# Kernel optimization log

Measured on AMD Instinct MI355X. Metric: run time of the kernel, lower is better.

Reference implementation:

```python
import jax, jax.numpy as jnp
import numpy as np

D_MODEL = 1024
N_HEADS = 16
D_K = D_MODEL // N_HEADS
B, S = 2, 2048


def setup_inputs() -> dict:
    key = jax.random.key(0)
    ks = jax.random.split(key, 5)
    sc = 1.0 / np.sqrt(D_MODEL)
    return {
        "x": jax.random.normal(ks[0], (B, S, D_MODEL), dtype=jnp.float32),
        "W_qkv": jax.random.normal(ks[1], (D_MODEL, 3 * D_MODEL), dtype=jnp.float32) * sc,
        "b_qkv": jnp.zeros((3 * D_MODEL,), dtype=jnp.float32),
        "W_out": jax.random.normal(ks[2], (D_MODEL, D_MODEL), dtype=jnp.float32) * sc,
        "b_out": jnp.zeros((D_MODEL,), dtype=jnp.float32),
    }


def reference(x, W_qkv, b_qkv, W_out, b_out):
    Bb, Ss, _ = x.shape
    qkv = x @ W_qkv + b_qkv                     # [B,S,3*D]
    qkv = qkv.reshape(Bb, Ss, 3, N_HEADS, D_K)
    qkv = jnp.transpose(qkv, (2, 0, 3, 1, 4))   # [3,B,H,S,Dk]
    q, k, v = qkv[0], qkv[1], qkv[2]
    scale = jnp.asarray(np.sqrt(D_K), dtype=x.dtype)
    attn = jnp.einsum('bhsd,bhtd->bhst', q, k) / scale  # [B,H,S,S]
    attn = jax.nn.softmax(attn, axis=-1)
    out = jnp.einsum('bhst,bhtd->bhsd', attn, v)        # [B,H,S,Dk]
    out = jnp.transpose(out, (0, 2, 1, 3)).reshape(Bb, Ss, D_MODEL)
    return out @ W_out + b_out
```

## Files before the change

### kernel.cpp

```cpp
#include <hip/hip_runtime.h>

typedef __bf16 bf16x8 __attribute__((ext_vector_type(8)));
typedef __bf16 bf16x4 __attribute__((ext_vector_type(4)));
typedef __bf16 bf16x2 __attribute__((ext_vector_type(2)));
typedef float f32x4 __attribute__((ext_vector_type(4)));
typedef unsigned short u16;
typedef unsigned short u16x4 __attribute__((ext_vector_type(4)));
typedef unsigned int u32;
typedef unsigned int u32x2 __attribute__((ext_vector_type(2)));
typedef unsigned int u32x4 __attribute__((ext_vector_type(4)));

__device__ __forceinline__ u16 f2bu(float f) {
  __bf16 h = (__bf16)f;
  return __builtin_bit_cast(u16, h);
}

__device__ __forceinline__ void gld16(const u16* g, const __bf16* lds) {
  __builtin_amdgcn_global_load_lds(
      (const __attribute__((address_space(1))) u32*)(uintptr_t)g,
      (__attribute__((address_space(3))) u32*)(u32)(uintptr_t)lds, 16, 0, 0);
}

__device__ __forceinline__ void tr_tile(const float* __restrict__ in, u16* __restrict__ out,
                                        int R, int C, int bx, int by, int tid) {
  __shared__ u16 t[64][65];
  int tx = tid & 63, ty = tid >> 6;
  int r0 = by * 64, c0 = bx * 64;
  for (int i = 0; i < 16; ++i)
    t[ty + i * 4][tx] = f2bu(in[(size_t)(r0 + ty + i * 4) * C + c0 + tx]);
  __syncthreads();
  for (int i = 0; i < 16; ++i)
    out[(size_t)(c0 + ty + i * 4) * R + r0 + tx] = t[tx][ty + i * 4];
}

__global__ __launch_bounds__(256) void prep(const float* __restrict__ Wqkv,
                                            u16* __restrict__ Wqkv_t,
                                            const float* __restrict__ Wout,
                                            u16* __restrict__ Wout_t,
                                            const float* __restrict__ x,
                                            u16* __restrict__ xb) {
  int id = blockIdx.x, tid = threadIdx.x;
  if (id < 768) {
    tr_tile(Wqkv, Wqkv_t, 1024, 3072, id % 48, id / 48, tid);
  } else if (id < 1024) {
    int id2 = id - 768;
    tr_tile(Wout, Wout_t, 1024, 1024, id2 % 16, id2 / 16, tid);
  } else {
    size_t i = ((size_t)(id - 1024) * 256 + tid) * 8;
    f32x4 a0 = *(const f32x4*)(x + i);
    f32x4 a1 = *(const f32x4*)(x + i + 4);
    bf16x8 v;
    for (int j = 0; j < 4; ++j) { v[j] = (__bf16)a0[j]; v[j + 4] = (__bf16)a1[j]; }
    *(bf16x8*)(xb + i) = v;
  }
}

template <int MODE, int TM, int TN, int MT, int NT, int XM, int XN>
__global__ __launch_bounds__(256) void gemm_bt(const u16* __restrict__ A,
                                               const u16* __restrict__ Bt,
                                               const float* __restrict__ bias,
                                               void* __restrict__ O0v,
                                               u16* __restrict__ O1,
                                               u16* __restrict__ O2,
                                               int M, int N, int K) {
  constexpr int NI = TM / 32;
  constexpr int NJ = TN / 32;
  constexpr int AE = TM * 32;
  constexpr int BE = TN * 32;
  __shared__ __bf16 smem[2 * (AE + BE)];

  int tid = threadIdx.x;
  int w = tid >> 6, lane = tid & 63, quad = lane >> 4, l16 = lane & 15;
  int wr = w >> 1, wc = w & 1;

  int id = blockIdx.x;
  int xcd = id & 7, s0i = id >> 3;
  int mg = xcd % (MT / XM), ng = xcd / (MT / XM);
  int sm = s0i % XM, sn = s0i / XM;
  int m0 = (mg * XM + sm) * TM, n0 = (ng * XN + sn) * TN;

  int srow = w * 16 + (lane >> 2);
  int sch = (lane & 3) ^ ((lane >> 3) & 3);
  const u16* Ag = A + (size_t)(m0 + srow) * K + sch * 8;
  const u16* Bg = Bt + (size_t)(n0 + srow) * K + sch * 8;

  int swl = (quad ^ ((l16 >> 1) & 3)) << 3;

  f32x4 acc[NI][NJ] = {};

#define GLD_STEP(c, kk)                                                          \
  {                                                                              \
    for (int p = 0; p < TM / 64; ++p)                                            \
      gld16(Ag + (size_t)p * 64 * K + (kk), smem + (c) * (AE + BE) + w * 512 + p * 2048); \
    for (int p = 0; p < TN / 64; ++p)                                            \
      gld16(Bg + (size_t)p * 64 * K + (kk), smem + (c) * (AE + BE) + AE + w * 512 + p * 2048); \
  }

  GLD_STEP(0, 0);
  int NS = K / 32;
  for (int s = 0; s < NS; ++s) {
    int cur = s & 1;
    __syncthreads();
    if (s + 1 < NS) GLD_STEP(1 - cur, (s + 1) * 32);
    const __bf16* Asub = smem + cur * (AE + BE);
    const __bf16* Bsub = Asub + AE;
    bf16x8 af[NI], bfr[NJ];
    for (int i = 0; i < NI; ++i)
      af[i] = *(const bf16x8*)(Asub + (wr * (TM / 2) + i * 16 + l16) * 32 + swl);
    for (int j = 0; j < NJ; ++j)
      bfr[j] = *(const bf16x8*)(Bsub + (wc * (TN / 2) + j * 16 + l16) * 32 + swl);
    for (int i = 0; i < NI; ++i)
      for (int j = 0; j < NJ; ++j)
        acc[i][j] = __builtin_amdgcn_mfma_f32_16x16x32_bf16(af[i], bfr[j], acc[i][j], 0, 0, 0);
  }
#undef GLD_STEP

  if (MODE == 0) {
    float* O0 = (float*)O0v;
    for (int j = 0; j < NJ; ++j) {
      int n = n0 + wc * (TN / 2) + j * 16 + l16;
      float bv = bias[n];
      for (int i = 0; i < NI; ++i) {
        int mb = m0 + wr * (TM / 2) + i * 16 + quad * 4;
        for (int r = 0; r < 4; ++r)
          O0[(size_t)(mb + r) * N + n] = acc[i][j][r] + bv;
      }
    }
  } else {
    u16* O0 = (u16*)O0v;
    constexpr float QSC = 0.125f * 1.44269504f;
    for (int j = 0; j < NJ; ++j) {
      int n = n0 + wc * (TN / 2) + j * 16 + l16;
      int which = n >> 10, rem = n & 1023, h = rem >> 6, d = rem & 63;
      float bv = bias[n];
      for (int i = 0; i < NI; ++i) {
        int m = m0 + wr * (TM / 2) + i * 16 + quad * 4;
        int b = m >> 11, s = m & 2047;
        if (which == 2) {
          u16x4 val;
          for (int r = 0; r < 4; ++r) val[r] = f2bu(acc[i][j][r] + bv);
          *(u16x4*)(O2 + (((size_t)(b * 16 + h)) * 64 + d) * 2048 + s) = val;
        } else {
          u16* Od = which ? O1 : O0;
          float sc = which ? 1.f : QSC;
          for (int r = 0; r < 4; ++r)
            Od[(((size_t)(b * 16 + h)) * 2048 + (s + r)) * 64 + d] = f2bu((acc[i][j][r] + bv) * sc);
        }
      }
    }
  }
}

__global__ __launch_bounds__(256, 2) void flash_attn(const u16* __restrict__ Q,
                                                     const u16* __restrict__ K,
                                                     const u16* __restrict__ Vt,
                                                     u16* __restrict__ AO) {
  constexpr int S = 2048;
  __shared__ __bf16 Ks[2][64 * 64];
  __shared__ __bf16 Vs[2][64 * 64];

  int bh = blockIdx.x, qbase = blockIdx.y * 128;
  int tid = threadIdx.x, w = tid >> 6, lane = tid & 63, quad = lane >> 4, l16 = lane & 15;

  const u16* Qh = Q + (size_t)bh * S * 64;
  const u16* Kh = K + (size_t)bh * S * 64;
  const u16* Vh = Vt + (size_t)bh * 64 * S;

  int qrowA = qbase + w * 32 + l16;
  int qrowB = qrowA + 16;
  bf16x8 qf0a = *(const bf16x8*)(Qh + (size_t)qrowA * 64 + quad * 8);
  bf16x8 qf1a = *(const bf16x8*)(Qh + (size_t)qrowA * 64 + 32 + quad * 8);
  bf16x8 qf0b = *(const bf16x8*)(Qh + (size_t)qrowB * 64 + quad * 8);
  bf16x8 qf1b = *(const bf16x8*)(Qh + (size_t)qrowB * 64 + 32 + quad * 8);

  bf16x8 vone;
#pragma unroll
  for (int j = 0; j < 8; ++j) vone[j] = (__bf16)1.0f;

  int r0s = tid >> 3, b0s = tid & 7;
  int r1s = r0s + 32;
  int ko0 = r0s * 64 + ((b0s ^ (r0s & 7)) << 3);
  int ko1 = r1s * 64 + ((b0s ^ (r1s & 7)) << 3);

  bf16x8 kr0, kr1, vr0, vr1;
#define LOAD_TILE(tb)                                                   \
  {                                                                     \
    kr0 = *(const bf16x8*)(Kh + (size_t)((tb) + r0s) * 64 + b0s * 8);   \
    kr1 = *(const bf16x8*)(Kh + (size_t)((tb) + r1s) * 64 + b0s * 8);   \
    vr0 = *(const bf16x8*)(Vh + (size_t)r0s * S + (tb) + b0s * 8);      \
    vr1 = *(const bf16x8*)(Vh + (size_t)r1s * S + (tb) + b0s * 8);      \
  }
#define STORE_TILE(c)                                                   \
  {                                                                     \
    *(bf16x8*)(&Ks[c][ko0]) = kr0;                                      \
    *(bf16x8*)(&Ks[c][ko1]) = kr1;                                      \
    *(bf16x8*)(&Vs[c][ko0]) = vr0;                                      \
    *(bf16x8*)(&Vs[c][ko1]) = vr1;                                      \
  }

  LOAD_TILE(0);
  STORE_TILE(0);
  LOAD_TILE(64);
  __syncthreads();

  f32x4 oA[4] = {};
  f32x4 oB[4] = {};
  f32x4 lfA = {};
  f32x4 lfB = {};
  int xr = l16 & 7;

  for (int it = 0; it < S / 64; ++it) {
    int c = it & 1;
    if (it + 1 < S / 64) STORE_TILE(1 - c);
    if (it + 2 < S / 64) LOAD_TILE((it + 2) * 64);

    u32 pwA[4][2], pwB[4][2];
#pragma unroll
    for (int nt = 0; nt < 4; ++nt) {
      const __bf16* kb = &Ks[c][(nt * 16 + l16) * 64];
      bf16x8 kf0 = *(const bf16x8*)(kb + ((quad ^ xr) << 3));
      bf16x8 kf1 = *(const bf16x8*)(kb + (((quad + 4) ^ xr) << 3));
      f32x4 ca = {0.f, 0.f, 0.f, 0.f};
      f32x4 cb = {0.f, 0.f, 0.f, 0.f};
      ca = __builtin_amdgcn_mfma_f32_16x16x32_bf16(kf0, qf0a, ca, 0, 0, 0);
      cb = __builtin_amdgcn_mfma_f32_16x16x32_bf16(kf0, qf0b, cb, 0, 0, 0);
      ca = __builtin_amdgcn_mfma_f32_16x16x32_bf16(kf1, qf1a, ca, 0, 0, 0);
      cb = __builtin_amdgcn_mfma_f32_16x16x32_bf16(kf1, qf1b, cb, 0, 0, 0);
      bf16x2 a01 = {(__bf16)__builtin_amdgcn_exp2f(ca[0]), (__bf16)__builtin_amdgcn_exp2f(ca[1])};
      bf16x2 a23 = {(__bf16)__builtin_amdgcn_exp2f(ca[2]), (__bf16)__builtin_amdgcn_exp2f(ca[3])};
      bf16x2 b01 = {(__bf16)__builtin_amdgcn_exp2f(cb[0]), (__bf16)__builtin_amdgcn_exp2f(cb[1])};
      bf16x2 b23 = {(__bf16)__builtin_amdgcn_exp2f(cb[2]), (__bf16)__builtin_amdgcn_exp2f(cb[3])};
      pwA[nt][0] = __builtin_bit_cast(u32, a01);
      pwA[nt][1] = __builtin_bit_cast(u32, a23);
      pwB[nt][0] = __builtin_bit_cast(u32, b01);
      pwB[nt][1] = __builtin_bit_cast(u32, b23);
    }

    bf16x8 pfA[2], pfB[2];
#pragma unroll
    for (int h = 0; h < 2; ++h) {
      u32 GA[2], HA[2], GB[2], HB[2];
#pragma unroll
      for (int w2 = 0; w2 < 2; ++w2) {
        u32x2 s1a = __builtin_amdgcn_permlane32_swap(pwA[2 * h][w2], pwA[2 * h + 1][w2], false, false);
        u32x2 s2a = __builtin_amdgcn_permlane16_swap(s1a[0], s1a[1], false, false);
        GA[w2] = s2a[0];
        HA[w2] = s2a[1];
        u32x2 s1b = __builtin_amdgcn_permlane32_swap(pwB[2 * h][w2], pwB[2 * h + 1][w2], false, false);
        u32x2 s2b = __builtin_amdgcn_permlane16_swap(s1b[0], s1b[1], false, false);
        GB[w2] = s2b[0];
        HB[w2] = s2b[1];
      }
      u32x4 pa = {GA[0], GA[1], HA[0], HA[1]};
      u32x4 pb = {GB[0], GB[1], HB[0], HB[1]};
      pfA[h] = __builtin_bit_cast(bf16x8, pa);
      pfB[h] = __builtin_bit_cast(bf16x8, pb);
    }

    lfA = __builtin_amdgcn_mfma_f32_16x16x32_bf16(pfA[0], vone, lfA, 0, 0, 0);
    lfA = __builtin_amdgcn_mfma_f32_16x16x32_bf16(pfA[1], vone, lfA, 0, 0, 0);
    lfB = __builtin_amdgcn_mfma_f32_16x16x32_bf16(pfB[0], vone, lfB, 0, 0, 0);
    lfB = __builtin_amdgcn_mfma_f32_16x16x32_bf16(pfB[1], vone, lfB, 0, 0, 0);

#pragma unroll
    for (int dt = 0; dt < 4; ++dt) {
      const __bf16* vb = &Vs[c][(dt * 16 + l16) * 64];
      bf16x8 v0 = *(const bf16x8*)(vb + ((quad ^ xr) << 3));
      bf16x8 v1 = *(const bf16x8*)(vb + (((quad + 4) ^ xr) << 3));
      oA[dt] = __builtin_amdgcn_mfma_f32_16x16x32_bf16(pfA[0], v0, oA[dt], 0, 0, 0);
      oB[dt] = __builtin_amdgcn_mfma_f32_16x16x32_bf16(pfB[0], v0, oB[dt], 0, 0, 0);
      oA[dt] = __builtin_amdgcn_mfma_f32_16x16x32_bf16(pfA[1], v1, oA[dt], 0, 0, 0);
      oB[dt] = __builtin_amdgcn_mfma_f32_16x16x32_bf16(pfB[1], v1, oB[dt], 0, 0, 0);
    }
    __syncthreads();
  }
#undef LOAD_TILE
#undef STORE_TILE

  float linvA[4], linvB[4];
#pragma unroll
  for (int r = 0; r < 4; ++r) {
    linvA[r] = 1.f / lfA[r];
    linvB[r] = 1.f / lfB[r];
  }

  int b = bh >> 4, h = bh & 15;
  for (int dt = 0; dt < 4; ++dt)
    for (int r = 0; r < 4; ++r) {
      int sA = qbase + w * 32 + quad * 4 + r;
      int sB = sA + 16;
      int d = dt * 16 + l16;
      AO[(((size_t)b * 2048 + sA) * 16 + h) * 64 + d] = f2bu(oA[dt][r] * linvA[r]);
      AO[(((size_t)b * 2048 + sB) * 16 + h) * 64 + d] = f2bu(oB[dt][r] * linvB[r]);
    }
}

extern "C" void kernel_launch(void* const* d_in, const int* in_sizes, int n_in,
                              void* d_out, int out_size, void* d_ws, size_t ws_size,
                              hipStream_t stream) {
  const float* x    = (const float*)d_in[0];
  const float* Wqkv = (const float*)d_in[1];
  const float* bqkv = (const float*)d_in[2];
  const float* Wout = (const float*)d_in[3];
  const float* bout = (const float*)d_in[4];
  float* out = (float*)d_out;

  u16* ws = (u16*)d_ws;
  size_t off = 0;
  u16* Wqkv_t = ws + off; off += (size_t)3072 * 1024;
  u16* Wout_t = ws + off; off += (size_t)1024 * 1024;
  u16* xb     = ws + off; off += (size_t)4096 * 1024;
  u16* Qb     = ws + off; off += (size_t)32 * 2048 * 64;
  u16* Kb     = ws + off; off += (size_t)32 * 2048 * 64;
  u16* Vtb    = ws + off; off += (size_t)32 * 2048 * 64;
  u16* AO     = xb;

  prep<<<dim3(3072), 256, 0, stream>>>(Wqkv, Wqkv_t, Wout, Wout_t, x, xb);
  gemm_bt<1, 128, 128, 32, 24, 8, 12><<<dim3(768), 256, 0, stream>>>(
      xb, Wqkv_t, bqkv, (void*)Qb, Kb, Vtb, 4096, 3072, 1024);
  flash_attn<<<dim3(32, 16), 256, 0, stream>>>(Qb, Kb, Vtb, AO);
  gemm_bt<0, 128, 64, 32, 16, 8, 8><<<dim3(512), 256, 0, stream>>>(
      AO, Wout_t, bout, (void*)out, nullptr, nullptr, 4096, 1024, 1024);
}
```

Baseline: 173.7 us.

## Split key range across two thread groups per attention block and merge in LDS

Each flash-attention block now runs 512 threads as two independent 256-thread groups. Each group streams half of the key/value sequence through its own double-buffered LDS tiles. At the end, group 1 writes its partial output accumulators and row sums to LDS, and group 0 adds them, normalizes and stores the result. The aim is to double the waves available per query tile for latency hiding and to halve the serial loop length. The costs are double the LDS footprint, an extra reduction pass with a block barrier, and a tighter register budget from the new launch bounds, which could cause spills.

```diff
diff --git a/kernel.cpp b/kernel.cpp
--- a/kernel.cpp
+++ b/kernel.cpp
@@ -151,20 +151,23 @@
   }
 }
 
-__global__ __launch_bounds__(256, 2) void flash_attn(const u16* __restrict__ Q,
+__global__ __launch_bounds__(512, 4) void flash_attn(const u16* __restrict__ Q,
                                                      const u16* __restrict__ K,
                                                      const u16* __restrict__ Vt,
                                                      u16* __restrict__ AO) {
   constexpr int S = 2048;
-  __shared__ __bf16 Ks[2][64 * 64];
-  __shared__ __bf16 Vs[2][64 * 64];
+  constexpr int HALF = S / 2;
+  constexpr int NIT = HALF / 64;
+  __shared__ __bf16 lds[2][2][2][64 * 64];
 
   int bh = blockIdx.x, qbase = blockIdx.y * 128;
-  int tid = threadIdx.x, w = tid >> 6, lane = tid & 63, quad = lane >> 4, l16 = lane & 15;
+  int tid = threadIdx.x;
+  int grp = tid >> 8, gtid = tid & 255;
+  int w = gtid >> 6, lane = tid & 63, quad = lane >> 4, l16 = lane & 15;
 
   const u16* Qh = Q + (size_t)bh * S * 64;
-  const u16* Kh = K + (size_t)bh * S * 64;
-  const u16* Vh = Vt + (size_t)bh * 64 * S;
+  const u16* Kh = K + (size_t)bh * S * 64 + (size_t)grp * HALF * 64;
+  const u16* Vh = Vt + (size_t)bh * 64 * S + grp * HALF;
 
   int qrowA = qbase + w * 32 + l16;
   int qrowB = qrowA + 16;
@@ -177,10 +180,13 @@
 #pragma unroll
   for (int j = 0; j < 8; ++j) vone[j] = (__bf16)1.0f;
 
-  int r0s = tid >> 3, b0s = tid & 7;
+  int r0s = gtid >> 3, b0s = gtid & 7;
   int r1s = r0s + 32;
   int ko0 = r0s * 64 + ((b0s ^ (r0s & 7)) << 3);
   int ko1 = r1s * 64 + ((b0s ^ (r1s & 7)) << 3);
+
+  __bf16* Ks0 = &lds[grp][0][0][0];
+  __bf16* Vs0 = &lds[grp][1][0][0];
 
   bf16x8 kr0, kr1, vr0, vr1;
 #define LOAD_TILE(tb)                                                   \
@@ -192,10 +198,10 @@
   }
 #define STORE_TILE(c)                                                   \
   {                                                                     \
-    *(bf16x8*)(&Ks[c][ko0]) = kr0;                                      \
-    *(bf16x8*)(&Ks[c][ko1]) = kr1;                                      \
-    *(bf16x8*)(&Vs[c][ko0]) = vr0;                                      \
-    *(bf16x8*)(&Vs[c][ko1]) = vr1;                                      \
+    *(bf16x8*)(Ks0 + (c) * 4096 + ko0) = kr0;                           \
+    *(bf16x8*)(Ks0 + (c) * 4096 + ko1) = kr1;                           \
+    *(bf16x8*)(Vs0 + (c) * 4096 + ko0) = vr0;                           \
+    *(bf16x8*)(Vs0 + (c) * 4096 + ko1) = vr1;                           \
   }
 
   LOAD_TILE(0);
@@ -209,15 +215,15 @@
   f32x4 lfB = {};
   int xr = l16 & 7;
 
-  for (int it = 0; it < S / 64; ++it) {
+  for (int it = 0; it < NIT; ++it) {
     int c = it & 1;
-    if (it + 1 < S / 64) STORE_TILE(1 - c);
-    if (it + 2 < S / 64) LOAD_TILE((it + 2) * 64);
+    if (it + 1 < NIT) STORE_TILE(1 - c);
+    if (it + 2 < NIT) LOAD_TILE((it + 2) * 64);
 
     u32 pwA[4][2], pwB[4][2];
 #pragma unroll
     for (int nt = 0; nt < 4; ++nt) {
-      const __bf16* kb = &Ks[c][(nt * 16 + l16) * 64];
+      const __bf16* kb = Ks0 + c * 4096 + (nt * 16 + l16) * 64;
       bf16x8 kf0 = *(const bf16x8*)(kb + ((quad ^ xr) << 3));
       bf16x8 kf1 = *(const bf16x8*)(kb + (((quad + 4) ^ xr) << 3));
       f32x4 ca = {0.f, 0.f, 0.f, 0.f};
@@ -264,7 +270,7 @@
 
 #pragma unroll
     for (int dt = 0; dt < 4; ++dt) {
-      const __bf16* vb = &Vs[c][(dt * 16 + l16) * 64];
+      const __bf16* vb = Vs0 + c * 4096 + (dt * 16 + l16) * 64;
       bf16x8 v0 = *(const bf16x8*)(vb + ((quad ^ xr) << 3));
       bf16x8 v1 = *(const bf16x8*)(vb + (((quad + 4) ^ xr) << 3));
       oA[dt] = __builtin_amdgcn_mfma_f32_16x16x32_bf16(pfA[0], v0, oA[dt], 0, 0, 0);
@@ -277,22 +283,41 @@
 #undef LOAD_TILE
 #undef STORE_TILE
 
-  float linvA[4], linvB[4];
-#pragma unroll
-  for (int r = 0; r < 4; ++r) {
-    linvA[r] = 1.f / lfA[r];
-    linvB[r] = 1.f / lfB[r];
-  }
-
-  int b = bh >> 4, h = bh & 15;
-  for (int dt = 0; dt < 4; ++dt)
+  float* mf = (float*)&lds[0][0][0][0];
+  if (grp) {
+    float* p = mf + (size_t)gtid * 41;
+#pragma unroll
+    for (int dt = 0; dt < 4; ++dt)
+#pragma unroll
+      for (int r = 0; r < 4; ++r) {
+        p[dt * 4 + r] = oA[dt][r];
+        p[16 + dt * 4 + r] = oB[dt][r];
+      }
+#pragma unroll
     for (int r = 0; r < 4; ++r) {
-      int sA = qbase + w * 32 + quad * 4 + r;
-      int sB = sA + 16;
-      int d = dt * 16 + l16;
-      AO[(((size_t)b * 2048 + sA) * 16 + h) * 64 + d] = f2bu(oA[dt][r] * linvA[r]);
-      AO[(((size_t)b * 2048 + sB) * 16 + h) * 64 + d] = f2bu(oB[dt][r] * linvB[r]);
-    }
+      p[32 + r] = lfA[r];
+      p[36 + r] = lfB[r];
+    }
+  }
+  __syncthreads();
+  if (!grp) {
+    const float* p = mf + (size_t)gtid * 41;
+    float linvA[4], linvB[4];
+#pragma unroll
+    for (int r = 0; r < 4; ++r) {
+      linvA[r] = 1.f / (lfA[r] + p[32 + r]);
+      linvB[r] = 1.f / (lfB[r] + p[36 + r]);
+    }
+    int b = bh >> 4, h = bh & 15;
+    for (int dt = 0; dt < 4; ++dt)
+      for (int r = 0; r < 4; ++r) {
+        int sA = qbase + w * 32 + quad * 4 + r;
+        int sB = sA + 16;
+        int d = dt * 16 + l16;
+        AO[(((size_t)b * 2048 + sA) * 16 + h) * 64 + d] = f2bu((oA[dt][r] + p[dt * 4 + r]) * linvA[r]);
+        AO[(((size_t)b * 2048 + sB) * 16 + h) * 64 + d] = f2bu((oB[dt][r] + p[16 + dt * 4 + r]) * linvB[r]);
+      }
+  }
 }
 
 extern "C" void kernel_launch(void* const* d_in, const int* in_sizes, int n_in,
@@ -318,7 +343,7 @@
   prep<<<dim3(3072), 256, 0, stream>>>(Wqkv, Wqkv_t, Wout, Wout_t, x, xb);
   gemm_bt<1, 128, 128, 32, 24, 8, 12><<<dim3(768), 256, 0, stream>>>(
       xb, Wqkv_t, bqkv, (void*)Qb, Kb, Vtb, 4096, 3072, 1024);
-  flash_attn<<<dim3(32, 16), 256, 0, stream>>>(Qb, Kb, Vtb, AO);
+  flash_attn<<<dim3(32, 16), 512, 0, stream>>>(Qb, Kb, Vtb, AO);
   gemm_bt<0, 128, 64, 32, 16, 8, 8><<<dim3(512), 256, 0, stream>>>(
       AO, Wout_t, bout, (void*)out, nullptr, nullptr, 4096, 1024, 1024);
 }
```

After: 174.0 us. Within noise of the previous version (+0.2%).
